# Kernel tuning notes

Measured on AMD Instinct MI355X. Metric: run time of the kernel, lower is better.

Reference implementation:

```python
import jax, jax.numpy as jnp
import numpy as np
from jax import lax

DIM = 1024
H = 16          # num_heads
HD = DIM // H   # head dim (qk and v identical)
D_INNER = 4     # fast-weight inner dim
CHUNK = 16
BASE_LR = 1e-3
KSZ = 4         # short conv kernel size


def short_conv(x, w):
    # x: (b, l, c), w: (c, KSZ). Depthwise causal conv + residual (as in ShortConvolution).
    xT = jnp.transpose(x, (0, 2, 1))  # (b, c, l)
    y = lax.conv_general_dilated(xT, w[:, None, :], window_strides=(1,),
                                 padding=[(KSZ - 1, 0)], feature_group_count=x.shape[-1],
                                 dimension_numbers=('NCH', 'OIH', 'NCH'))
    return jnp.transpose(y + xT, (0, 2, 1))


def l2norm(x):
    # interpret torch.norm(..., dim=-1) as L2 normalization over head dim (required for shape consistency)
    return x / jnp.linalg.norm(x, axis=-1, keepdims=True)


def attn(q, k, v):
    # flash_attn_func equivalent: non-causal softmax attention, scale 1/sqrt(d)
    # q: (b, D, h, d), k/v: (b, L, h, d)
    s = jnp.einsum('bqhd,bkhd->bhqk', q, k) / jnp.sqrt(jnp.asarray(q.shape[-1], q.dtype))
    p = jax.nn.softmax(s, axis=-1)
    return jnp.einsum('bhqk,bkhd->bqhd', p, v)


def setup_inputs() -> dict:
    key = jax.random.key(0)
    ks = jax.random.split(key, 12)
    b, l = 4, 4096
    s = 1.0 / np.sqrt(DIM)
    return {
        'hidden_states': jax.random.normal(ks[0], (b, l, DIM), jnp.float32),
        'Wq': jax.random.normal(ks[1], (DIM, DIM), jnp.float32) * s,
        'Wk': jax.random.normal(ks[2], (DIM, DIM), jnp.float32) * s,
        'Wv': jax.random.normal(ks[3], (DIM, DIM), jnp.float32) * s,
        'Wlr': jax.random.normal(ks[4], (H * 2, DIM), jnp.float32) * s,
        'Wg': jax.random.normal(ks[5], (DIM, DIM), jnp.float32) * s,
        'Wo': jax.random.normal(ks[6], (DIM, DIM), jnp.float32) * s,
        'cq': jax.random.normal(ks[7], (DIM, KSZ), jnp.float32) * 0.1,
        'ck': jax.random.normal(ks[8], (DIM, KSZ), jnp.float32) * 0.1,
        'cv': jax.random.normal(ks[9], (DIM, KSZ), jnp.float32) * 0.1,
        'W_in_init': jax.random.normal(ks[10], (1, D_INNER, H, HD), jnp.float32) / np.sqrt(HD),
        'W_out_init': jax.random.normal(ks[11], (1, D_INNER, H, HD), jnp.float32) / np.sqrt(D_INNER),
        'ln_g': jnp.ones((HD,), jnp.float32),
        'ln_b': jnp.zeros((HD,), jnp.float32),
    }


def _forward(hidden_states, Wq, Wk, Wv, Wlr, Wg, Wo, cq, ck, cv, W_in_init, W_out_init, ln_g, ln_b):
    b, l, _ = hidden_states.shape
    q = l2norm(jax.nn.silu(short_conv(hidden_states @ Wq.T, cq)).reshape(b, l, H, HD))
    k = l2norm(jax.nn.silu(short_conv(hidden_states @ Wk.T, ck)).reshape(b, l, H, HD))
    v = jax.nn.silu(short_conv(hidden_states @ Wv.T, cv)).reshape(b, l, H, HD)
    lr = jax.nn.softplus(hidden_states @ Wlr.T + BASE_LR).reshape(b, l, H, 2)

    nc = l // CHUNK
    to_chunks = lambda x: x.reshape(b, nc, CHUNK, H, -1).transpose(1, 0, 2, 3, 4)
    qc, kc, vc, lrc = map(to_chunks, (q, k, v, lr))

    W_in0 = jnp.broadcast_to(W_in_init, (b, D_INNER, H, HD))
    W_out0 = jnp.broadcast_to(W_out_init, (b, D_INNER, H, HD))
    mask = jnp.tril(jnp.ones((CHUNK, CHUNK), jnp.float32))  # causal within chunk (diag kept)

    def step(carry, xs):
        W_in, W_out = carry
        q_t, k_t, v_t, lr_t = xs  # (b, CHUNK, H, d) / lr (b, CHUNK, H, 2)
        k_h = jax.nn.softmax(jnp.einsum('blhd,bDhd->blhD', k_t, W_in), axis=-1) * lr_t[..., 1:]
        q_h = jax.nn.softmax(jnp.einsum('blhd,bDhd->blhD', q_t, W_in), axis=-1)
        qk = jnp.einsum('bqhD,bkhD->bhqk', q_h, k_h) * mask
        o_t = jnp.einsum('bqhD,bDhd->bqhd', q_h, W_out) + jnp.einsum('bhqk,bkhd->bqhd', qk, v_t)
        W_out = W_out + jnp.einsum('bnhD,bnhd->bDhd', k_h, v_t)
        lr_in = lr_t[:, :1, :, 0:1]    # (b,1,h,1)
        lr_out = lr_t[:, :1, :, 1:2]
        # two nested test-time gradient steps via attention
        for _ in range(2):
            g_out = -attn(W_in, k_t, v_t)
            g_in = -attn(W_out, v_t, k_t)
            W_in = W_in - lr_in * g_in
            W_out = W_out - lr_out * g_out
        return (W_in, W_out), o_t

    _, o = lax.scan(step, (W_in0, W_out0), (qc, kc, vc, lrc))
    o = o.transpose(1, 0, 2, 3, 4).reshape(b, l, H, HD)

    mu = o.mean(-1, keepdims=True)
    var = ((o - mu) ** 2).mean(-1, keepdims=True)
    o = (o - mu) / jnp.sqrt(var + 1e-5) * ln_g + ln_b
    o = o.reshape(b, l, DIM)
    gate = hidden_states @ Wg.T
    return (o * gate) @ Wo.T


def reference(hidden_states, Wq, Wk, Wv, Wlr, Wg, Wo, cq, ck, cv, W_in_init, W_out_init, ln_g, ln_b):
    return _forward(hidden_states, Wq, Wk, Wv, Wlr, Wg, Wo, cq, ck, cv, W_in_init, W_out_init, ln_g, ln_b)
```

## Files before the change

kernel.cpp:

```cpp
#include <hip/hip_runtime.h>
#include <cstdint>
#include <cstddef>

#define DIM    1024
#define NH     16
#define HD     64
#define CHUNK_ 16
#define SEQ    4096
#define BATCH  4
#define NROWS  (BATCH * SEQ)
#define NCHUNK (SEQ / CHUNK_)
#define SEG    64
#define NSEG   (SEQ / SEG)

using bf16x8 = __attribute__((ext_vector_type(8))) short;
using f32x4  = __attribute__((ext_vector_type(4))) float;
typedef union { bf16x8 v; uint32_t u[4]; } B8;

#define MFMA16(a, b, c) __builtin_amdgcn_mfma_f32_16x16x32_bf16((a), (b), (c), 0, 0, 0)

__device__ __forceinline__ ushort f2bf(float f) {
    uint32_t u = __float_as_uint(f);
    u += 0x7FFFu + ((u >> 16) & 1u);
    return (ushort)(u >> 16);
}
__device__ __forceinline__ uint32_t pack2(float a, float b) {
    return (uint32_t)f2bf(a) | ((uint32_t)f2bf(b) << 16);
}
__device__ __forceinline__ float b2f(ushort u) {
    return __uint_as_float(((uint32_t)u) << 16);
}
__device__ __forceinline__ float dot4(const float4 a, const float4 b) {
    return a.x*b.x + a.y*b.y + a.z*b.z + a.w*b.w;
}

template <int N>
__device__ __forceinline__ float ror16(float x) {
    return __int_as_float(__builtin_amdgcn_update_dpp(
        0, __float_as_int(x), 0x120 + N, 0xF, 0xF, true));
}
__device__ __forceinline__ float dppsum16(float x) {
    x += ror16<1>(x); x += ror16<2>(x);
    x += ror16<4>(x); x += ror16<8>(x);
    return x;
}

#define SYNC() asm volatile("" ::: "memory")

__device__ __forceinline__ void gl_lds16(const void* g, void* l) {
    __builtin_amdgcn_global_load_lds(
        (const __attribute__((address_space(1))) void*)g,
        (__attribute__((address_space(3))) void*)l, 16, 0, 0);
}

__global__ __launch_bounds__(256)
void f2b_kernel(const float* __restrict__ in, ushort* __restrict__ out, int n8)
{
    int i = blockIdx.x * 256 + threadIdx.x;
    const int stride = gridDim.x * 256;
    for (; i < n8; i += stride) {
        float4 a = *(const float4*)&in[(size_t)i * 8];
        float4 b = *(const float4*)&in[(size_t)i * 8 + 4];
        uint4 u;
        u.x = pack2(a.x, a.y); u.y = pack2(a.z, a.w);
        u.z = pack2(b.x, b.y); u.w = pack2(b.z, b.w);
        *(uint4*)&out[(size_t)i * 8] = u;
    }
}

__global__ __launch_bounds__(256)
void f2b5_kernel(const float* __restrict__ w0, const float* __restrict__ w1,
                 const float* __restrict__ w2, const float* __restrict__ w3,
                 const float* __restrict__ w4, ushort* __restrict__ out)
{
    const int W8 = DIM * DIM / 8;
    const int w  = blockIdx.x >> 7;
    const float* src = (w == 0) ? w0 : (w == 1) ? w1 : (w == 2) ? w2
                     : (w == 3) ? w3 : w4;
    ushort* dst = out + (size_t)w * DIM * DIM;
    for (int i = (blockIdx.x & 127) * 256 + threadIdx.x; i < W8; i += 128 * 256) {
        float4 a = *(const float4*)&src[(size_t)i * 8];
        float4 b = *(const float4*)&src[(size_t)i * 8 + 4];
        uint4 u;
        u.x = pack2(a.x, a.y); u.y = pack2(a.z, a.w);
        u.z = pack2(b.x, b.y); u.w = pack2(b.z, b.w);
        *(uint4*)&dst[(size_t)i * 8] = u;
    }
}

#define GEMM_LDS_BODY(EPILOG)                                                  \
    __shared__ ushort As[128][64];                                             \
    __shared__ ushort Bs[128][64];                                             \
    const int tid  = threadIdx.x, wave = tid >> 6, lane = tid & 63;            \
    const int m0   = blockIdx.y * 128, n0 = blockIdx.x * 128;                  \
    const int lo   = lane & 15, kg = lane >> 4;                                \
    const int wm   = (wave >> 1) * 64, wn = (wave & 1) * 64;                   \
    const int rin  = lane >> 3, sl = lane & 7;                                 \
    const int sb   = 32 * wave;                                                \
    f32x4 acc[4][4];                                                           \
    _Pragma("unroll")                                                          \
    for (int i = 0; i < 4; ++i)                                                \
        _Pragma("unroll")                                                      \
        for (int j = 0; j < 4; ++j) acc[i][j] = (f32x4){0.f, 0.f, 0.f, 0.f};   \
    const int swz = lo & 7;                                                    \
    for (int kt = 0; kt < K; kt += 64) {                                       \
        __syncthreads();                                                       \
        _Pragma("unroll")                                                      \
        for (int i = 0; i < 4; ++i) {                                          \
            const int row = sb + 8 * i + rin;                                  \
            const int gs  = sl ^ (row & 7);                                    \
            gl_lds16(A + (size_t)(m0 + row) * K + kt + gs * 8,                 \
                     &As[sb + 8 * i][0]);                                      \
            gl_lds16(B + (size_t)(n0 + row) * K + kt + gs * 8,                 \
                     &Bs[sb + 8 * i][0]);                                      \
        }                                                                      \
        __syncthreads();                                                       \
        bf16x8 af[2][4], bfr[2][4];                                            \
        _Pragma("unroll")                                                      \
        for (int kk = 0; kk < 2; ++kk)                                         \
            _Pragma("unroll")                                                  \
            for (int m = 0; m < 4; ++m) {                                      \
                const int s = (kk * 4 + kg) ^ swz;                             \
                af[kk][m]  = *(const bf16x8*)&As[wm + m * 16 + lo][s * 8];     \
                bfr[kk][m] = *(const bf16x8*)&Bs[wn + m * 16 + lo][s * 8];     \
            }                                                                  \
        _Pragma("unroll")                                                      \
        for (int kk = 0; kk < 2; ++kk)                                         \
            _Pragma("unroll")                                                  \
            for (int mt = 0; mt < 4; ++mt)                                     \
                _Pragma("unroll")                                              \
                for (int nt = 0; nt < 4; ++nt)                                 \
                    acc[mt][nt] = MFMA16(af[kk][mt], bfr[kk][nt], acc[mt][nt]);\
    }                                                                          \
    const int col = lane & 15, r4 = (lane >> 4) * 4;                           \
    _Pragma("unroll")                                                          \
    for (int mt = 0; mt < 4; ++mt)                                             \
        _Pragma("unroll")                                                      \
        for (int nt = 0; nt < 4; ++nt)                                         \
            _Pragma("unroll")                                                  \
            for (int j = 0; j < 4; ++j) {                                      \
                size_t idx = (size_t)(m0 + wm + mt * 16 + r4 + j) * DIM +      \
                             n0 + wn + nt * 16 + col;                          \
                EPILOG;                                                        \
            }

__global__ __launch_bounds__(256)
void gemm_lds_b16o(const ushort* __restrict__ A, const ushort* __restrict__ B,
                   ushort* __restrict__ C, int K)
{
    GEMM_LDS_BODY(C[idx] = f2bf(acc[mt][nt][j]))
}

__global__ __launch_bounds__(256)
void gemm_lds_f32o(const ushort* __restrict__ A, const ushort* __restrict__ B,
                   float* __restrict__ C, int K)
{
    GEMM_LDS_BODY(C[idx] = acc[mt][nt][j])
}

__global__ __launch_bounds__(256)
void lr_kernel(const float* __restrict__ hs, const float* __restrict__ Wlr,
               float* __restrict__ LR)
{
    __shared__ float row[DIM];
    const int r = blockIdx.x;
    const int t = threadIdx.x;
    *(float4*)&row[t * 4] = *(const float4*)&hs[(size_t)r * DIM + t * 4];
    __syncthreads();

    const int o = t >> 3;
    const int p = t & 7;
    const float* w = Wlr + (size_t)o * DIM + p * 128;
    const float* x = row + p * 128;
    float acc = 0.f;
#pragma unroll
    for (int i = 0; i < 32; ++i) {
        float4 xv = *(const float4*)(x + i * 4);
        float4 wv = *(const float4*)(w + i * 4);
        acc += dot4(xv, wv);
    }
    acc += __shfl_xor(acc, 1);
    acc += __shfl_xor(acc, 2);
    acc += __shfl_xor(acc, 4);
    if (p == 0) {
        float xx = acc + 0.001f;
        LR[(size_t)r * 32 + o] = (xx > 20.f) ? xx : log1pf(expf(xx));
    }
}

__global__ __launch_bounds__(256)
void halo_save(const ushort* __restrict__ Q, const ushort* __restrict__ K,
               const ushort* __restrict__ V, ushort* __restrict__ HALO)
{
    int idx = blockIdx.x;
    int tn  = idx / (BATCH * (NSEG - 1) * 3);
    int rem = idx - tn * (BATCH * (NSEG - 1) * 3);
    int b   = rem / ((NSEG - 1) * 3);
    int rem2= rem - b * ((NSEG - 1) * 3);
    int s   = rem2 / 3 + 1;
    int j   = rem2 - (s - 1) * 3;

    const ushort* buf = (tn == 0) ? Q : ((tn == 1) ? K : V);
    size_t src = ((size_t)(b * SEQ + s * SEG - 3 + j)) * DIM + threadIdx.x * 4;
    size_t dst = ((size_t)((tn * BATCH + b) * NSEG + s) * 3 + j) * DIM + threadIdx.x * 4;
    *(uint2*)&HALO[dst] = *(const uint2*)&buf[src];
}

__global__ __launch_bounds__(256)
void conv_inplace(ushort* __restrict__ Q, ushort* __restrict__ K,
                  ushort* __restrict__ V, const ushort* __restrict__ HALO,
                  const float* __restrict__ cq, const float* __restrict__ ck,
                  const float* __restrict__ cv)
{
    const int wid  = (blockIdx.x << 2) + (threadIdx.x >> 6);
    const int lane = threadIdx.x & 63;
    const int tn   = wid >> 12;
    const int rem  = wid & 4095;
    const int b    = rem >> 10;
    const int rem2 = rem & 1023;
    const int h    = rem2 >> 6;
    const int s    = rem2 & 63;
    const int c    = (h << 6) + lane;

    ushort* buf = (tn == 0) ? Q : ((tn == 1) ? K : V);
    const float* cw = (tn == 0) ? cq : ((tn == 1) ? ck : cv);
    float4 w4 = *(const float4*)(cw + (c << 2));

    float xm3 = 0.f, xm2 = 0.f, xm1 = 0.f;
    if (s > 0) {
        size_t hb = ((size_t)((tn * BATCH + b) * NSEG + s) * 3) * DIM + c;
        xm3 = b2f(HALO[hb]);
        xm2 = b2f(HALO[hb + DIM]);
        xm1 = b2f(HALO[hb + 2 * DIM]);
    }

    size_t base = ((size_t)(b * SEQ + s * SEG)) * DIM + c;
    float x_next = b2f(buf[base]);
#pragma unroll 4
    for (int i = 0; i < SEG; ++i) {
        float x = x_next;
        if (i < SEG - 1) x_next = b2f(buf[base + (size_t)(i + 1) * DIM]);
        float y = xm3 * w4.x + xm2 * w4.y + xm1 * w4.z + x * w4.w + x;
        y = y / (1.f + __expf(-y));
        if (tn < 2) {
            float n2 = y * y;
#pragma unroll
            for (int m = 1; m < 64; m <<= 1) n2 += __shfl_xor(n2, m);
            y *= rsqrtf(n2);
        }
        buf[base + (size_t)i * DIM] = f2bf(y);
        xm3 = xm2; xm2 = xm1; xm1 = x;
    }
}

__global__ __launch_bounds__(64)
void scan_kernel(const ushort* QP, const ushort* __restrict__ KP,
                 const ushort* __restrict__ VP, const float* __restrict__ LRb,
                 const float* __restrict__ GATE,
                 const float* __restrict__ Wi0, const float* __restrict__ Wo0,
                 const float* __restrict__ lng, const float* __restrict__ lnb,
                 ushort* OB)
{
    const int bh = blockIdx.x, b = bh >> 4, h = bh & 15;
    const int t  = threadIdx.x, lo = t & 15, g = t >> 4;

    __shared__ ushort KA2[2][16][72], QA2[2][16][72], VA2[2][16][72];
    __shared__ float  sG2[2][16][68];
    __shared__ ushort KT2[2][64][24];
    __shared__ ushort VT2[2][64][40];
    __shared__ ushort WiA[16][72], WoA[16][72];
    __shared__ ushort QKT[16][32], KH[16][32];

    for (int i = t; i < 16 * 72; i += 64) { ((ushort*)WiA)[i] = 0; ((ushort*)WoA)[i] = 0; }
    for (int i = t; i < 2 * 64 * 24; i += 64) ((ushort*)KT2)[i] = 0;
    for (int i = t; i < 2 * 64 * 40; i += 64) ((ushort*)VT2)[i] = 0;
    for (int i = t; i < 16 * 32; i += 64) { ((ushort*)QKT)[i] = 0; ((ushort*)KH)[i] = 0; }

    f32x4 wiC[4], woC[4];
#pragma unroll
    for (int n = 0; n < 4; ++n) { wiC[n] = (f32x4){0,0,0,0}; woC[n] = (f32x4){0,0,0,0}; }
    if (g == 0) {
#pragma unroll
        for (int n = 0; n < 4; ++n)
#pragma unroll
            for (int D = 0; D < 4; ++D) {
                float wi = Wi0[((size_t)D * NH + h) * HD + 16 * n + lo];
                float wo = Wo0[((size_t)D * NH + h) * HD + 16 * n + lo];
                wiC[n][D] = wi; woC[n][D] = wo;
                WiA[D][16 * n + lo] = f2bf(wi);
                WoA[D][16 * n + lo] = f2bf(wo);
                VT2[0][16 * n + lo][16 + D] = f2bf(wo);
            }
    }
    __builtin_amdgcn_wave_barrier();
    SYNC();

    float lnGr[4], lnBr[4];
#pragma unroll
    for (int n = 0; n < 4; ++n) { lnGr[n] = lng[16 * n + lo]; lnBr[n] = lnb[16 * n + lo]; }

    const int rowb = b * SEQ;
    const ushort* QPh = QP + h * 64;
    const ushort* KPh = KP + h * 64;
    const ushort* VPh = VP + h * 64;
    const float*  GPh = GATE + h * 64;
    ushort*       OBh = OB + h * 64;

    uint2 pq[4], pk[4], pv[4];
    float4 pg[4];
    float plr_q, plr_i, plr_o;

    {
#pragma unroll
        for (int i = 0; i < 4; ++i) {
            size_t go = (size_t)(rowb + i * 4 + g) * DIM + 4 * lo;
            pq[i] = *(const uint2*)&QPh[go];
            pk[i] = *(const uint2*)&KPh[go];
            pv[i] = *(const uint2*)&VPh[go];
            pg[i] = *(const float4*)&GPh[go];
        }
        plr_q = LRb[(size_t)(rowb + lo) * 32 + h * 2 + 1];
        plr_i = LRb[(size_t)rowb * 32 + h * 2];
        plr_o = LRb[(size_t)rowb * 32 + h * 2 + 1];
    }

    auto STAGE = [&](int nb) {
#pragma unroll
        for (int i = 0; i < 4; ++i) {
            const int row = i * 4 + g;
            *(float4*)&sG2[nb][row][4 * lo] = pg[i];
            *(uint2*)&QA2[nb][row][4 * lo] = pq[i];
            *(uint2*)&KA2[nb][row][4 * lo] = pk[i];
            *(uint2*)&VA2[nb][row][4 * lo] = pv[i];
            uint2 uk = pk[i], uv = pv[i];
            KT2[nb][4 * lo + 0][row] = (ushort)(uk.x & 0xFFFF);
            KT2[nb][4 * lo + 1][row] = (ushort)(uk.x >> 16);
            KT2[nb][4 * lo + 2][row] = (ushort)(uk.y & 0xFFFF);
            KT2[nb][4 * lo + 3][row] = (ushort)(uk.y >> 16);
            VT2[nb][4 * lo + 0][row] = (ushort)(uv.x & 0xFFFF);
            VT2[nb][4 * lo + 1][row] = (ushort)(uv.x >> 16);
            VT2[nb][4 * lo + 2][row] = (ushort)(uv.y & 0xFFFF);
            VT2[nb][4 * lo + 3][row] = (ushort)(uv.y >> 16);
        }
    };

    STAGE(0);
    SYNC();

    const f32x4 z4 = (f32x4){0.f, 0.f, 0.f, 0.f};
    const uint32_t pmsk = (g < 2) ? 0xFFFFFFFFu : 0u;
    const int L0 = (lo + 32 * g) & 63, L1 = (L0 + 16) & 63;

    for (int c = 0; c < NCHUNK; ++c) {
        const int rb  = rowb + c * CHUNK_;
        const int cur = c & 1, nxt = cur ^ 1;
        ushort (*KAc)[72] = KA2[cur];
        ushort (*QAc)[72] = QA2[cur];
        ushort (*VAc)[72] = VA2[cur];
        float  (*sGc)[68] = sG2[cur];
        ushort (*KTc)[24] = KT2[cur];
        ushort (*VTc)[40] = VT2[cur];

        const float lr1    = plr_q;
        const float lr_in  = plr_i;
        const float lr_out = plr_o;

        if (c + 1 < NCHUNK) {
            const int rb2 = rb + CHUNK_;
#pragma unroll
            for (int i = 0; i < 4; ++i) {
                size_t go = (size_t)(rb2 + i * 4 + g) * DIM + 4 * lo;
                pq[i] = *(const uint2*)&QPh[go];
                pk[i] = *(const uint2*)&KPh[go];
                pv[i] = *(const uint2*)&VPh[go];
                pg[i] = *(const float4*)&GPh[go];
            }
            plr_q = LRb[(size_t)(rb2 + lo) * 32 + h * 2 + 1];
            plr_i = LRb[(size_t)rb2 * 32 + h * 2];
            plr_o = LRb[(size_t)rb2 * 32 + h * 2 + 1];
        }

        bf16x8 xWi0 = *(const bf16x8*)&WiA[lo][g * 8];
        bf16x8 xWi1 = *(const bf16x8*)&WiA[lo][g * 8 + 32];
        f32x4 cK = MFMA16(xWi0, *(const bf16x8*)&KAc[lo][g * 8], z4);
        cK = MFMA16(xWi1, *(const bf16x8*)&KAc[lo][g * 8 + 32], cK);
        f32x4 cQ = MFMA16(xWi0, *(const bf16x8*)&QAc[lo][g * 8], z4);
        cQ = MFMA16(xWi1, *(const bf16x8*)&QAc[lo][g * 8 + 32], cQ);

        float mK = fmaxf(fmaxf(cK[0], cK[1]), fmaxf(cK[2], cK[3]));
        float ek0 = __expf(cK[0] - mK), ek1 = __expf(cK[1] - mK);
        float ek2 = __expf(cK[2] - mK), ek3 = __expf(cK[3] - mK);
        float ivk = lr1 / (ek0 + ek1 + ek2 + ek3);
        float kh0 = ek0 * ivk, kh1 = ek1 * ivk, kh2 = ek2 * ivk, kh3 = ek3 * ivk;

        float mQ = fmaxf(fmaxf(cQ[0], cQ[1]), fmaxf(cQ[2], cQ[3]));
        float eq0 = __expf(cQ[0] - mQ), eq1 = __expf(cQ[1] - mQ);
        float eq2 = __expf(cQ[2] - mQ), eq3 = __expf(cQ[3] - mQ);
        float ivq = 1.f / (eq0 + eq1 + eq2 + eq3);
        float qh0 = eq0 * ivq, qh1 = eq1 * ivq, qh2 = eq2 * ivq, qh3 = eq3 * ivq;

        B8 aQh, bKh;
        aQh.u[0] = aQh.u[1] = aQh.u[2] = aQh.u[3] = 0;
        bKh.u[0] = bKh.u[1] = bKh.u[2] = bKh.u[3] = 0;
        if (g == 0) {
            aQh.u[0] = pack2(qh0, qh1); aQh.u[1] = pack2(qh2, qh3);
            bKh.u[0] = pack2(kh0, kh1); bKh.u[1] = pack2(kh2, kh3);
        }
        f32x4 cQK = MFMA16(aQh.v, bKh.v, z4);

#pragma unroll
        for (int r = 0; r < 4; ++r) {
            const int q = 4 * g + r;
            QKT[q][lo] = (lo <= q) ? f2bf(cQK[r]) : (ushort)0;
        }
        if (g == 0) {
            QKT[lo][16] = f2bf(qh0); QKT[lo][17] = f2bf(qh1);
            QKT[lo][18] = f2bf(qh2); QKT[lo][19] = f2bf(qh3);
            KH[0][lo] = f2bf(kh0); KH[1][lo] = f2bf(kh1);
            KH[2][lo] = f2bf(kh2); KH[3][lo] = f2bf(kh3);
        }
        SYNC();

        bf16x8 aO = *(const bf16x8*)&QKT[lo][g * 8];
        f32x4 oA[4];
#pragma unroll
        for (int n = 0; n < 4; ++n)
            oA[n] = MFMA16(aO, *(const bf16x8*)&VTc[16 * n + lo][g * 8], z4);
#pragma unroll
        for (int r = 0; r < 4; ++r) {
            float s1 = oA[0][r] + oA[1][r] + oA[2][r] + oA[3][r];
            float s2 = oA[0][r] * oA[0][r] + oA[1][r] * oA[1][r] +
                       oA[2][r] * oA[2][r] + oA[3][r] * oA[3][r];
            s1 = dppsum16(s1); s2 = dppsum16(s2);
            float mu = s1 * (1.f / 64.f);
            float rstd = rsqrtf(s2 * (1.f / 64.f) - mu * mu + 1e-5f);
            const int q = 4 * g + r;
#pragma unroll
            for (int n = 0; n < 4; ++n) {
                float val = (oA[n][r] - mu) * rstd * lnGr[n] + lnBr[n];
                val *= sGc[q][16 * n + lo];
                OBh[(size_t)(rb + q) * DIM + 16 * n + lo] = f2bf(val);
            }
        }
        {
            bf16x8 aKH = *(const bf16x8*)&KH[lo][g * 8];
#pragma unroll
            for (int n = 0; n < 4; ++n)
                woC[n] = MFMA16(aKH, *(const bf16x8*)&VTc[16 * n + lo][g * 8], woC[n]);
        }
        if (g == 0) {
#pragma unroll
            for (int n = 0; n < 4; ++n)
#pragma unroll
                for (int D = 0; D < 4; ++D)
                    WoA[D][16 * n + lo] = f2bf(woC[n][D]);
        }
        SYNC();

#pragma unroll
        for (int it = 0; it < 2; ++it) {
            bf16x8 aK0 = *(const bf16x8*)&KAc[lo][g * 8];
            bf16x8 aK1 = *(const bf16x8*)&KAc[lo][g * 8 + 32];
            bf16x8 aV0 = *(const bf16x8*)&VAc[lo][g * 8];
            bf16x8 aV1 = *(const bf16x8*)&VAc[lo][g * 8 + 32];
            bf16x8 bWi0 = *(const bf16x8*)&WiA[lo][g * 8];
            bf16x8 bWi1 = *(const bf16x8*)&WiA[lo][g * 8 + 32];
            bf16x8 bWo0 = *(const bf16x8*)&WoA[lo][g * 8];
            bf16x8 bWo1 = *(const bf16x8*)&WoA[lo][g * 8 + 32];
            f32x4 s0T = MFMA16(aK0, bWi0, z4);
            s0T = MFMA16(aK1, bWi1, s0T);
            f32x4 s1T = MFMA16(aV0, bWo0, z4);
            s1T = MFMA16(aV1, bWo1, s1T);

            float x0[4], x1[4];
#pragma unroll
            for (int r = 0; r < 4; ++r) {
                x0[r] = s0T[r] * 0.125f;
                x1[r] = s1T[r] * 0.125f;
            }
            float m0 = fmaxf(fmaxf(x0[0], x0[1]), fmaxf(x0[2], x0[3]));
            float m1 = fmaxf(fmaxf(x1[0], x1[1]), fmaxf(x1[2], x1[3]));
            m0 = fmaxf(m0, __shfl_xor(m0, 16)); m0 = fmaxf(m0, __shfl_xor(m0, 32));
            m1 = fmaxf(m1, __shfl_xor(m1, 16)); m1 = fmaxf(m1, __shfl_xor(m1, 32));
            float e0[4], e1[4];
#pragma unroll
            for (int r = 0; r < 4; ++r) {
                e0[r] = __expf(x0[r] - m0);
                e1[r] = __expf(x1[r] - m1);
            }
            float su0 = e0[0] + e0[1] + e0[2] + e0[3];
            float su1 = e1[0] + e1[1] + e1[2] + e1[3];
            su0 += __shfl_xor(su0, 16); su0 += __shfl_xor(su0, 32);
            su1 += __shfl_xor(su1, 16); su1 += __shfl_xor(su1, 32);
            const float w0 = lr_out / su0;
            const float w1 = lr_in / su1;

            uint32_t p00 = pack2(e0[0] * w0, e0[1] * w0);
            uint32_t p01 = pack2(e0[2] * w0, e0[3] * w0);
            uint32_t p10 = pack2(e1[0] * w1, e1[1] * w1);
            uint32_t p11 = pack2(e1[2] * w1, e1[3] * w1);
            B8 aP0, aP1;
            aP0.u[0] = (uint32_t)__shfl((int)p00, L0) & pmsk;
            aP0.u[1] = (uint32_t)__shfl((int)p01, L0) & pmsk;
            aP0.u[2] = (uint32_t)__shfl((int)p00, L1) & pmsk;
            aP0.u[3] = (uint32_t)__shfl((int)p01, L1) & pmsk;
            aP1.u[0] = (uint32_t)__shfl((int)p10, L0) & pmsk;
            aP1.u[1] = (uint32_t)__shfl((int)p11, L0) & pmsk;
            aP1.u[2] = (uint32_t)__shfl((int)p10, L1) & pmsk;
            aP1.u[3] = (uint32_t)__shfl((int)p11, L1) & pmsk;

#pragma unroll
            for (int n = 0; n < 4; ++n) {
                woC[n] = MFMA16(aP0.v, *(const bf16x8*)&VTc[16 * n + lo][g * 8], woC[n]);
                wiC[n] = MFMA16(aP1.v, *(const bf16x8*)&KTc[16 * n + lo][g * 8], wiC[n]);
            }

            if (it == 1 && c + 1 < NCHUNK) STAGE(nxt);

            if (g == 0) {
#pragma unroll
                for (int n = 0; n < 4; ++n)
#pragma unroll
                    for (int D = 0; D < 4; ++D) {
                        WiA[D][16 * n + lo] = f2bf(wiC[n][D]);
                        WoA[D][16 * n + lo] = f2bf(woC[n][D]);
                        if (it == 1) VT2[nxt][16 * n + lo][16 + D] = f2bf(woC[n][D]);
                    }
            }
            SYNC();
        }
    }
}

extern "C" void kernel_launch(void* const* d_in, const int* in_sizes, int n_in,
                              void* d_out, int out_size, void* d_ws, size_t ws_size,
                              hipStream_t stream)
{
    const float* hs  = (const float*)d_in[0];
    const float* Wq  = (const float*)d_in[1];
    const float* Wk  = (const float*)d_in[2];
    const float* Wv  = (const float*)d_in[3];
    const float* Wlr = (const float*)d_in[4];
    const float* Wg  = (const float*)d_in[5];
    const float* Wo  = (const float*)d_in[6];
    const float* cq  = (const float*)d_in[7];
    const float* ck  = (const float*)d_in[8];
    const float* cv  = (const float*)d_in[9];
    const float* Wi0 = (const float*)d_in[10];
    const float* Wo0 = (const float*)d_in[11];
    const float* lng = (const float*)d_in[12];
    const float* lnb = (const float*)d_in[13];

    ushort* Qb   = (ushort*)d_ws;
    ushort* Kb   = Qb + (size_t)NROWS * DIM;
    ushort* Vb   = Kb + (size_t)NROWS * DIM;
    ushort* hsb  = Vb + (size_t)NROWS * DIM;
    ushort* Wqb  = hsb + (size_t)NROWS * DIM;
    ushort* Wkb  = Wqb + (size_t)DIM * DIM;
    ushort* Wvb  = Wkb + (size_t)DIM * DIM;
    ushort* Wgb  = Wvb + (size_t)DIM * DIM;
    ushort* Wob  = Wgb + (size_t)DIM * DIM;
    ushort* HALO = Wob + (size_t)DIM * DIM;
    float*  LRb  = (float*)(HALO + (size_t)3 * BATCH * NSEG * 3 * DIM);
    float*  GATE = (float*)d_out;
    ushort* OBUF = hsb;

    dim3 blk(256);

    f2b_kernel<<<2048, blk, 0, stream>>>(hs, hsb, NROWS * DIM / 8);
    f2b5_kernel<<<640, blk, 0, stream>>>(Wq, Wk, Wv, Wg, Wo, Wqb);

    gemm_lds_b16o<<<dim3(8, 128), blk, 0, stream>>>(hsb, Wqb, Qb, 1024);
    gemm_lds_b16o<<<dim3(8, 128), blk, 0, stream>>>(hsb, Wkb, Kb, 1024);
    gemm_lds_b16o<<<dim3(8, 128), blk, 0, stream>>>(hsb, Wvb, Vb, 1024);
    gemm_lds_f32o<<<dim3(8, 128), blk, 0, stream>>>(hsb, Wgb, GATE, 1024);

    lr_kernel<<<NROWS, blk, 0, stream>>>(hs, Wlr, LRb);

    halo_save<<<3 * BATCH * (NSEG - 1) * 3, blk, 0, stream>>>(Qb, Kb, Vb, HALO);
    conv_inplace<<<(3 * BATCH * NH * NSEG) / 4, blk, 0, stream>>>(Qb, Kb, Vb, HALO,
                                                                  cq, ck, cv);

    scan_kernel<<<BATCH * NH, dim3(64), 0, stream>>>(Qb, Kb, Vb, LRb, GATE,
                                                     Wi0, Wo0, lng, lnb, OBUF);

    gemm_lds_f32o<<<dim3(8, 128), blk, 0, stream>>>(OBUF, Wob, (float*)d_out, 1024);
}
```

Before: 1.737 ms.

## Fuse Q/K/V/gate projections into one GEMM and parallelize conv per row

```diff
diff --git a/kernel.cpp b/kernel.cpp
--- a/kernel.cpp
+++ b/kernel.cpp
@@ -10,8 +10,6 @@
 #define BATCH  4
 #define NROWS  (BATCH * SEQ)
 #define NCHUNK (SEQ / CHUNK_)
-#define SEG    64
-#define NSEG   (SEQ / SEG)
 
 using bf16x8 = __attribute__((ext_vector_type(8))) short;
 using f32x4  = __attribute__((ext_vector_type(4))) float;
@@ -88,74 +86,140 @@
     }
 }
 
-#define GEMM_LDS_BODY(EPILOG)                                                  \
-    __shared__ ushort As[128][64];                                             \
-    __shared__ ushort Bs[128][64];                                             \
-    const int tid  = threadIdx.x, wave = tid >> 6, lane = tid & 63;            \
-    const int m0   = blockIdx.y * 128, n0 = blockIdx.x * 128;                  \
-    const int lo   = lane & 15, kg = lane >> 4;                                \
-    const int wm   = (wave >> 1) * 64, wn = (wave & 1) * 64;                   \
-    const int rin  = lane >> 3, sl = lane & 7;                                 \
-    const int sb   = 32 * wave;                                                \
-    f32x4 acc[4][4];                                                           \
-    _Pragma("unroll")                                                          \
-    for (int i = 0; i < 4; ++i)                                                \
-        _Pragma("unroll")                                                      \
-        for (int j = 0; j < 4; ++j) acc[i][j] = (f32x4){0.f, 0.f, 0.f, 0.f};   \
-    const int swz = lo & 7;                                                    \
-    for (int kt = 0; kt < K; kt += 64) {                                       \
-        __syncthreads();                                                       \
-        _Pragma("unroll")                                                      \
-        for (int i = 0; i < 4; ++i) {                                          \
-            const int row = sb + 8 * i + rin;                                  \
-            const int gs  = sl ^ (row & 7);                                    \
-            gl_lds16(A + (size_t)(m0 + row) * K + kt + gs * 8,                 \
-                     &As[sb + 8 * i][0]);                                      \
-            gl_lds16(B + (size_t)(n0 + row) * K + kt + gs * 8,                 \
-                     &Bs[sb + 8 * i][0]);                                      \
-        }                                                                      \
-        __syncthreads();                                                       \
-        bf16x8 af[2][4], bfr[2][4];                                            \
-        _Pragma("unroll")                                                      \
-        for (int kk = 0; kk < 2; ++kk)                                         \
-            _Pragma("unroll")                                                  \
-            for (int m = 0; m < 4; ++m) {                                      \
-                const int s = (kk * 4 + kg) ^ swz;                             \
-                af[kk][m]  = *(const bf16x8*)&As[wm + m * 16 + lo][s * 8];     \
-                bfr[kk][m] = *(const bf16x8*)&Bs[wn + m * 16 + lo][s * 8];     \
-            }                                                                  \
-        _Pragma("unroll")                                                      \
-        for (int kk = 0; kk < 2; ++kk)                                         \
-            _Pragma("unroll")                                                  \
-            for (int mt = 0; mt < 4; ++mt)                                     \
-                _Pragma("unroll")                                              \
-                for (int nt = 0; nt < 4; ++nt)                                 \
-                    acc[mt][nt] = MFMA16(af[kk][mt], bfr[kk][nt], acc[mt][nt]);\
-    }                                                                          \
-    const int col = lane & 15, r4 = (lane >> 4) * 4;                           \
-    _Pragma("unroll")                                                          \
-    for (int mt = 0; mt < 4; ++mt)                                             \
-        _Pragma("unroll")                                                      \
-        for (int nt = 0; nt < 4; ++nt)                                         \
-            _Pragma("unroll")                                                  \
-            for (int j = 0; j < 4; ++j) {                                      \
-                size_t idx = (size_t)(m0 + wm + mt * 16 + r4 + j) * DIM +      \
-                             n0 + wn + nt * 16 + col;                          \
-                EPILOG;                                                        \
-            }
-
 __global__ __launch_bounds__(256)
-void gemm_lds_b16o(const ushort* __restrict__ A, const ushort* __restrict__ B,
-                   ushort* __restrict__ C, int K)
-{
-    GEMM_LDS_BODY(C[idx] = f2bf(acc[mt][nt][j]))
+void gemm_proj(const ushort* __restrict__ A, const ushort* __restrict__ B,
+               ushort* __restrict__ Cb, float* __restrict__ GATE, int K)
+{
+    __shared__ ushort As[128][64];
+    __shared__ ushort Bs[128][64];
+
+    const int nwg  = gridDim.x * gridDim.y;
+    const int bid0 = blockIdx.y * gridDim.x + blockIdx.x;
+    const int qq   = nwg >> 3;
+    const int sbid = (bid0 & 7) * qq + (bid0 >> 3);
+    const int bx   = sbid % gridDim.x, by = sbid / gridDim.x;
+
+    const int tid  = threadIdx.x, wave = tid >> 6, lane = tid & 63;
+    const int m0   = by * 128, n0g = bx * 128;
+    const int tt   = n0g >> 10, n0 = n0g & 1023;
+    const int lo   = lane & 15, kg = lane >> 4;
+    const int wm   = (wave >> 1) * 64, wn = (wave & 1) * 64;
+    const int rin  = lane >> 3, sl = lane & 7;
+    const int sb   = 32 * wave;
+    const int swz  = lo & 7;
+
+    f32x4 acc[4][4];
+#pragma unroll
+    for (int i = 0; i < 4; ++i)
+#pragma unroll
+        for (int j = 0; j < 4; ++j) acc[i][j] = (f32x4){0.f, 0.f, 0.f, 0.f};
+
+    for (int kt = 0; kt < K; kt += 64) {
+        __syncthreads();
+#pragma unroll
+        for (int i = 0; i < 4; ++i) {
+            const int row = sb + 8 * i + rin;
+            const int gs  = sl ^ (row & 7);
+            gl_lds16(A + (size_t)(m0 + row) * K + kt + gs * 8, &As[sb + 8 * i][0]);
+            gl_lds16(B + (size_t)(n0g + row) * K + kt + gs * 8, &Bs[sb + 8 * i][0]);
+        }
+        __syncthreads();
+
+        bf16x8 af[2][4], bfr[2][4];
+#pragma unroll
+        for (int kk = 0; kk < 2; ++kk)
+#pragma unroll
+            for (int m = 0; m < 4; ++m) {
+                const int s = (kk * 4 + kg) ^ swz;
+                af[kk][m]  = *(const bf16x8*)&As[wm + m * 16 + lo][s * 8];
+                bfr[kk][m] = *(const bf16x8*)&Bs[wn + m * 16 + lo][s * 8];
+            }
+#pragma unroll
+        for (int kk = 0; kk < 2; ++kk)
+#pragma unroll
+            for (int mt = 0; mt < 4; ++mt)
+#pragma unroll
+                for (int nt = 0; nt < 4; ++nt)
+                    acc[mt][nt] = MFMA16(af[kk][mt], bfr[kk][nt], acc[mt][nt]);
+    }
+
+    const int col = lane & 15, r4 = (lane >> 4) * 4;
+    if (tt < 3) {
+        ushort* C = Cb + (size_t)tt * NROWS * DIM;
+#pragma unroll
+        for (int mt = 0; mt < 4; ++mt)
+#pragma unroll
+            for (int nt = 0; nt < 4; ++nt)
+#pragma unroll
+                for (int j = 0; j < 4; ++j)
+                    C[(size_t)(m0 + wm + mt * 16 + r4 + j) * DIM +
+                      n0 + wn + nt * 16 + col] = f2bf(acc[mt][nt][j]);
+    } else {
+#pragma unroll
+        for (int mt = 0; mt < 4; ++mt)
+#pragma unroll
+            for (int nt = 0; nt < 4; ++nt)
+#pragma unroll
+                for (int j = 0; j < 4; ++j)
+                    GATE[(size_t)(m0 + wm + mt * 16 + r4 + j) * DIM +
+                         n0 + wn + nt * 16 + col] = acc[mt][nt][j];
+    }
 }
 
 __global__ __launch_bounds__(256)
 void gemm_lds_f32o(const ushort* __restrict__ A, const ushort* __restrict__ B,
                    float* __restrict__ C, int K)
 {
-    GEMM_LDS_BODY(C[idx] = acc[mt][nt][j])
+    __shared__ ushort As[128][64];
+    __shared__ ushort Bs[128][64];
+    const int tid  = threadIdx.x, wave = tid >> 6, lane = tid & 63;
+    const int m0   = blockIdx.y * 128, n0 = blockIdx.x * 128;
+    const int lo   = lane & 15, kg = lane >> 4;
+    const int wm   = (wave >> 1) * 64, wn = (wave & 1) * 64;
+    const int rin  = lane >> 3, sl = lane & 7;
+    const int sb   = 32 * wave;
+    f32x4 acc[4][4];
+#pragma unroll
+    for (int i = 0; i < 4; ++i)
+#pragma unroll
+        for (int j = 0; j < 4; ++j) acc[i][j] = (f32x4){0.f, 0.f, 0.f, 0.f};
+    const int swz = lo & 7;
+    for (int kt = 0; kt < K; kt += 64) {
+        __syncthreads();
+#pragma unroll
+        for (int i = 0; i < 4; ++i) {
+            const int row = sb + 8 * i + rin;
+            const int gs  = sl ^ (row & 7);
+            gl_lds16(A + (size_t)(m0 + row) * K + kt + gs * 8, &As[sb + 8 * i][0]);
+            gl_lds16(B + (size_t)(n0 + row) * K + kt + gs * 8, &Bs[sb + 8 * i][0]);
+        }
+        __syncthreads();
+        bf16x8 af[2][4], bfr[2][4];
+#pragma unroll
+        for (int kk = 0; kk < 2; ++kk)
+#pragma unroll
+            for (int m = 0; m < 4; ++m) {
+                const int s = (kk * 4 + kg) ^ swz;
+                af[kk][m]  = *(const bf16x8*)&As[wm + m * 16 + lo][s * 8];
+                bfr[kk][m] = *(const bf16x8*)&Bs[wn + m * 16 + lo][s * 8];
+            }
+#pragma unroll
+        for (int kk = 0; kk < 2; ++kk)
+#pragma unroll
+            for (int mt = 0; mt < 4; ++mt)
+#pragma unroll
+                for (int nt = 0; nt < 4; ++nt)
+                    acc[mt][nt] = MFMA16(af[kk][mt], bfr[kk][nt], acc[mt][nt]);
+    }
+    const int col = lane & 15, r4 = (lane >> 4) * 4;
+#pragma unroll
+    for (int mt = 0; mt < 4; ++mt)
+#pragma unroll
+        for (int nt = 0; nt < 4; ++nt)
+#pragma unroll
+            for (int j = 0; j < 4; ++j)
+                C[(size_t)(m0 + wm + mt * 16 + r4 + j) * DIM +
+                  n0 + wn + nt * 16 + col] = acc[mt][nt][j];
 }
 
 __global__ __launch_bounds__(256)
@@ -189,68 +253,42 @@
 }
 
 __global__ __launch_bounds__(256)
-void halo_save(const ushort* __restrict__ Q, const ushort* __restrict__ K,
-               const ushort* __restrict__ V, ushort* __restrict__ HALO)
-{
-    int idx = blockIdx.x;
-    int tn  = idx / (BATCH * (NSEG - 1) * 3);
-    int rem = idx - tn * (BATCH * (NSEG - 1) * 3);
-    int b   = rem / ((NSEG - 1) * 3);
-    int rem2= rem - b * ((NSEG - 1) * 3);
-    int s   = rem2 / 3 + 1;
-    int j   = rem2 - (s - 1) * 3;
-
-    const ushort* buf = (tn == 0) ? Q : ((tn == 1) ? K : V);
-    size_t src = ((size_t)(b * SEQ + s * SEG - 3 + j)) * DIM + threadIdx.x * 4;
-    size_t dst = ((size_t)((tn * BATCH + b) * NSEG + s) * 3 + j) * DIM + threadIdx.x * 4;
-    *(uint2*)&HALO[dst] = *(const uint2*)&buf[src];
-}
-
-__global__ __launch_bounds__(256)
-void conv_inplace(ushort* __restrict__ Q, ushort* __restrict__ K,
-                  ushort* __restrict__ V, const ushort* __restrict__ HALO,
-                  const float* __restrict__ cq, const float* __restrict__ ck,
-                  const float* __restrict__ cv)
+void conv_par(const ushort* __restrict__ Qp, const ushort* __restrict__ Kp,
+              const ushort* __restrict__ Vp,
+              ushort* __restrict__ Q, ushort* __restrict__ K,
+              ushort* __restrict__ V,
+              const float* __restrict__ cq, const float* __restrict__ ck,
+              const float* __restrict__ cv)
 {
     const int wid  = (blockIdx.x << 2) + (threadIdx.x >> 6);
     const int lane = threadIdx.x & 63;
-    const int tn   = wid >> 12;
-    const int rem  = wid & 4095;
-    const int b    = rem >> 10;
-    const int rem2 = rem & 1023;
-    const int h    = rem2 >> 6;
-    const int s    = rem2 & 63;
+    const int tn   = wid / (NROWS * NH);
+    const int rem  = wid - tn * (NROWS * NH);
+    const int h    = rem >> 14;
+    const int r    = rem & (NROWS - 1);
+    const int l    = r & (SEQ - 1);
     const int c    = (h << 6) + lane;
 
-    ushort* buf = (tn == 0) ? Q : ((tn == 1) ? K : V);
-    const float* cw = (tn == 0) ? cq : ((tn == 1) ? ck : cv);
+    const ushort* src = (tn == 0) ? Qp : ((tn == 1) ? Kp : Vp);
+    const float*  cw  = (tn == 0) ? cq : ((tn == 1) ? ck : cv);
     float4 w4 = *(const float4*)(cw + (c << 2));
 
-    float xm3 = 0.f, xm2 = 0.f, xm1 = 0.f;
-    if (s > 0) {
-        size_t hb = ((size_t)((tn * BATCH + b) * NSEG + s) * 3) * DIM + c;
-        xm3 = b2f(HALO[hb]);
-        xm2 = b2f(HALO[hb + DIM]);
-        xm1 = b2f(HALO[hb + 2 * DIM]);
-    }
-
-    size_t base = ((size_t)(b * SEQ + s * SEG)) * DIM + c;
-    float x_next = b2f(buf[base]);
-#pragma unroll 4
-    for (int i = 0; i < SEG; ++i) {
-        float x = x_next;
-        if (i < SEG - 1) x_next = b2f(buf[base + (size_t)(i + 1) * DIM]);
-        float y = xm3 * w4.x + xm2 * w4.y + xm1 * w4.z + x * w4.w + x;
-        y = y / (1.f + __expf(-y));
-        if (tn < 2) {
-            float n2 = y * y;
-#pragma unroll
-            for (int m = 1; m < 64; m <<= 1) n2 += __shfl_xor(n2, m);
-            y *= rsqrtf(n2);
-        }
-        buf[base + (size_t)i * DIM] = f2bf(y);
-        xm3 = xm2; xm2 = xm1; xm1 = x;
-    }
+    const size_t base = (size_t)r * DIM + c;
+    float x0  = b2f(src[base]);
+    float xm1 = (l >= 1) ? b2f(src[base - DIM])     : 0.f;
+    float xm2 = (l >= 2) ? b2f(src[base - 2 * DIM]) : 0.f;
+    float xm3 = (l >= 3) ? b2f(src[base - 3 * DIM]) : 0.f;
+
+    float y = xm3 * w4.x + xm2 * w4.y + xm1 * w4.z + x0 * w4.w + x0;
+    y = y / (1.f + __expf(-y));
+    if (tn < 2) {
+        float n2 = y * y;
+#pragma unroll
+        for (int m = 1; m < 64; m <<= 1) n2 += __shfl_xor(n2, m);
+        y *= rsqrtf(n2);
+    }
+    ushort* dst = (tn == 0) ? Q : ((tn == 1) ? K : V);
+    dst[base] = f2bf(y);
 }
 
 __global__ __launch_bounds__(64)
@@ -551,35 +589,30 @@
     const float* lng = (const float*)d_in[12];
     const float* lnb = (const float*)d_in[13];
 
-    ushort* Qb   = (ushort*)d_ws;
-    ushort* Kb   = Qb + (size_t)NROWS * DIM;
+    ushort* Qpre = (ushort*)d_ws;
+    ushort* Kpre = Qpre + (size_t)NROWS * DIM;
+    ushort* Vpre = Kpre + (size_t)NROWS * DIM;
+    ushort* Kb   = Vpre + (size_t)NROWS * DIM;
     ushort* Vb   = Kb + (size_t)NROWS * DIM;
     ushort* hsb  = Vb + (size_t)NROWS * DIM;
     ushort* Wqb  = hsb + (size_t)NROWS * DIM;
-    ushort* Wkb  = Wqb + (size_t)DIM * DIM;
-    ushort* Wvb  = Wkb + (size_t)DIM * DIM;
-    ushort* Wgb  = Wvb + (size_t)DIM * DIM;
-    ushort* Wob  = Wgb + (size_t)DIM * DIM;
-    ushort* HALO = Wob + (size_t)DIM * DIM;
-    float*  LRb  = (float*)(HALO + (size_t)3 * BATCH * NSEG * 3 * DIM);
+    ushort* Wob  = Wqb + (size_t)4 * DIM * DIM;
+    float*  LRb  = (float*)(Wob + (size_t)DIM * DIM);
     float*  GATE = (float*)d_out;
-    ushort* OBUF = hsb;
+    ushort* Qb   = hsb;
+    ushort* OBUF = Qpre;
 
     dim3 blk(256);
 
     f2b_kernel<<<2048, blk, 0, stream>>>(hs, hsb, NROWS * DIM / 8);
     f2b5_kernel<<<640, blk, 0, stream>>>(Wq, Wk, Wv, Wg, Wo, Wqb);
 
-    gemm_lds_b16o<<<dim3(8, 128), blk, 0, stream>>>(hsb, Wqb, Qb, 1024);
-    gemm_lds_b16o<<<dim3(8, 128), blk, 0, stream>>>(hsb, Wkb, Kb, 1024);
-    gemm_lds_b16o<<<dim3(8, 128), blk, 0, stream>>>(hsb, Wvb, Vb, 1024);
-    gemm_lds_f32o<<<dim3(8, 128), blk, 0, stream>>>(hsb, Wgb, GATE, 1024);
+    gemm_proj<<<dim3(32, 128), blk, 0, stream>>>(hsb, Wqb, Qpre, GATE, 1024);
 
     lr_kernel<<<NROWS, blk, 0, stream>>>(hs, Wlr, LRb);
 
-    halo_save<<<3 * BATCH * (NSEG - 1) * 3, blk, 0, stream>>>(Qb, Kb, Vb, HALO);
-    conv_inplace<<<(3 * BATCH * NH * NSEG) / 4, blk, 0, stream>>>(Qb, Kb, Vb, HALO,
-                                                                  cq, ck, cv);
+    conv_par<<<(3 * NROWS * NH) / 4, blk, 0, stream>>>(Qpre, Kpre, Vpre,
+                                                       Qb, Kb, Vb, cq, ck, cv);
 
     scan_kernel<<<BATCH * NH, dim3(64), 0, stream>>>(Qb, Kb, Vb, LRb, GATE,
                                                      Wi0, Wo0, lng, lnb, OBUF);
```

Result: slower. 1.848 ms (+6.4%).
